# Performance work log

Measured on AMD Instinct MI355X. Metric: run time of the kernel, lower is better.

Reference implementation:

```python
import jax, jax.numpy as jnp
import numpy as np

HID = 256
POS_FREQ = 10
DIR_FREQ = 4
POS_ENC = 3 * (2 * POS_FREQ + 1)   # 63
DIR_ENC = 3 * (2 * DIR_FREQ + 1)   # 27
N_PTS = 262144


def _posenc(x, num_freq):
    freqs = (2.0 ** jnp.arange(num_freq)).astype(x.dtype)      # [F]
    xf = x[..., None, :] * freqs[:, None]                       # [..., F, D]
    sc = jnp.stack([jnp.sin(xf), jnp.cos(xf)], axis=-2)         # [..., F, 2, D]
    return jnp.concatenate([x, sc.reshape(*x.shape[:-1], -1)], axis=-1)


def _linear_init(key, fan_in, fan_out):
    kw, kb = jax.random.split(key)
    s = 1.0 / np.sqrt(fan_in)
    W = jax.random.uniform(kw, (fan_in, fan_out), jnp.float32, -s, s)
    b = jax.random.uniform(kb, (fan_out,), jnp.float32, -s, s)
    return W, b


def setup_inputs() -> dict:
    key = jax.random.key(0)
    ks = jax.random.split(key, 16)
    inp = {
        "positions": jax.random.normal(ks[0], (N_PTS, 3), jnp.float32),
        "directions": jax.random.normal(ks[1], (N_PTS, 3), jnp.float32),
    }
    W, b = _linear_init(ks[2], POS_ENC, HID)
    inp["W_in"], inp["b_in"] = W, b
    # 7 hidden layers; layer index 4 takes skip concat (HID + POS_ENC)
    for i in range(7):
        fan_in = HID + POS_ENC if i == 4 else HID
        W, b = _linear_init(ks[3 + i], fan_in, HID)
        inp[f"W_h{i}"], inp[f"b_h{i}"] = W, b
    W, b = _linear_init(ks[10], HID, HID + 1)
    inp["W_out"], inp["b_out"] = W, b
    W, b = _linear_init(ks[11], HID + DIR_ENC, HID // 2)
    inp["W_r1"], inp["b_r1"] = W, b
    W, b = _linear_init(ks[12], HID // 2, 3)
    inp["W_r2"], inp["b_r2"] = W, b
    return inp


def _forward(positions, directions, W_in, b_in, hidden_params, W_out, b_out,
             W_r1, b_r1, W_r2, b_r2):
    pe = _posenc(positions, POS_FREQ)    # [N, 63]
    de = _posenc(directions, DIR_FREQ)   # [N, 27]
    h = jax.nn.relu(pe @ W_in + b_in)    # [N, 256]
    for i, (W, b) in enumerate(hidden_params):
        if i == 4:
            h = jnp.concatenate([h, pe], axis=-1)  # skip connection [N, 319]
        h = jax.nn.relu(h @ W + b)
    out = h @ W_out + b_out                      # [N, 257]
    features = out[..., :HID]                    # [N, 256]
    density = jax.nn.relu(out[..., HID:HID + 1])  # [N, 1]
    rgb_in = jnp.concatenate([features, de], axis=-1)  # [N, 283]
    rgb = jax.nn.sigmoid(jax.nn.relu(rgb_in @ W_r1 + b_r1) @ W_r2 + b_r2)  # [N, 3]
    return rgb, density


def reference(positions, directions, W_in, b_in,
              W_h0, b_h0, W_h1, b_h1, W_h2, b_h2, W_h3, b_h3,
              W_h4, b_h4, W_h5, b_h5, W_h6, b_h6,
              W_out, b_out, W_r1, b_r1, W_r2, b_r2):
    hidden = [(W_h0, b_h0), (W_h1, b_h1), (W_h2, b_h2), (W_h3, b_h3),
              (W_h4, b_h4), (W_h5, b_h5), (W_h6, b_h6)]
    return _forward(positions, directions, W_in, b_in, hidden,
                    W_out, b_out, W_r1, b_r1, W_r2, b_r2)
```

## Files before the change

kernel.cpp:

```cpp
#include <hip/hip_runtime.h>
#include <math.h>

#define NPTS 262144
#define MT 128

typedef __attribute__((ext_vector_type(8))) short bf16x8;
typedef __attribute__((ext_vector_type(4))) float f32x4;
typedef __attribute__((ext_vector_type(16))) float f32x16;
typedef __attribute__((ext_vector_type(2))) unsigned int u32x2;

#if defined(__has_builtin)
#if __has_builtin(__builtin_amdgcn_cvt_pk_bf16_f32)
#define HAVE_CVT_PK_BF16 1
#endif
#endif

__device__ __forceinline__ short f2bf(float f) {
    union { float f; unsigned u; } v; v.f = f;
    unsigned r = v.u + 0x7fffu + ((v.u >> 16) & 1u);
    return (short)(r >> 16);
}
__device__ __forceinline__ unsigned pk2(float a, float b) {
#ifdef HAVE_CVT_PK_BF16
    auto r = __builtin_amdgcn_cvt_pk_bf16_f32(a, b);
    unsigned u; __builtin_memcpy(&u, &r, 4);
    return u;
#else
    return ((unsigned)(unsigned short)f2bf(a)) |
           ((unsigned)(unsigned short)f2bf(b) << 16);
#endif
}

__device__ __forceinline__ void barrier_lds() {
    asm volatile("s_waitcnt lgkmcnt(0)" ::: "memory");
    __builtin_amdgcn_s_barrier();
}

#define OFF_IN   0
#define SZ_IN    (64*256)
#define OFF_H0   (OFF_IN + SZ_IN)
#define SZ_H     (256*256)
#define OFF_H1   (OFF_H0 + SZ_H)
#define OFF_H2   (OFF_H1 + SZ_H)
#define OFF_H3   (OFF_H2 + SZ_H)
#define OFF_H4   (OFF_H3 + SZ_H)
#define SZ_H4    (320*256)
#define OFF_H5   (OFF_H4 + SZ_H4)
#define OFF_H6   (OFF_H5 + SZ_H)
#define OFF_OUT  (OFF_H6 + SZ_H)
#define SZ_OUTM  (256*256)
#define OFF_OUTD (OFF_OUT + SZ_OUTM)
#define SZ_OUTD  (256*16)
#define OFF_R1   (OFF_OUTD + SZ_OUTD)
#define SZ_R1    (288*128)
#define OFF_R2   (OFF_R1 + SZ_R1)
#define SZ_R2    (128*16)
#define WS_TOTAL (OFF_R2 + SZ_R2)

struct PrepP { const float* W[11]; short* ws; };

__global__ __launch_bounds__(256) void prep_all(PrepP pp) {
    int i = blockIdx.x * 256 + threadIdx.x;
    if (i >= WS_TOTAL) return;
    const int offs[13] = {OFF_IN, OFF_H0, OFF_H1, OFF_H2, OFF_H3, OFF_H4,
                          OFF_H5, OFF_H6, OFF_OUT, OFF_OUTD, OFF_R1, OFF_R2,
                          WS_TOTAL};
    const int wsrc[12] = {0,1,2,3,4,5,6,7,8,8,9,10};
    const int Ks[12]   = {63,256,256,256,256,319,256,256,256,256,283,128};
    const int Nsrc[12] = {256,256,256,256,256,256,256,256,257,257,128,3};
    int seg = 0;
    while (i >= offs[seg + 1]) seg++;
    int li = i - offs[seg];
    int j = li & 7, L = (li >> 3) & 63, tile = li >> 9;
    const float* W = pp.W[wsrc[seg]];
    float v = 0.f;
    if (seg == 9) {
        int k = tile * 32 + ((L >> 4) << 3) + j;
        if (k < 256 && (L & 15) == 0) v = W[k * 257 + 256];
    } else if (seg == 11) {
        int k = tile * 32 + ((L >> 4) << 3) + j;
        int n = L & 15;
        if (k < 128 && n < 3) v = W[k * 3 + n];
    } else {
        int nNb = (seg == 10) ? 4 : 8;
        int nb = tile % nNb, kt = tile / nNb;
        int k = kt * 16 + ((L >> 5) << 3) + j;
        int n = nb * 32 + (L & 31);
        if (k < Ks[seg]) v = W[k * Nsrc[seg] + n];
    }
    pp.ws[i] = f2bf(v);
}

struct Params {
    const float *pos, *dir;
    const float *b_in, *b_h0, *b_h1, *b_h2, *b_h3, *b_h4, *b_h5, *b_h6;
    const float *b_out, *b_r1, *b_r2;
    const short *w;
    float *out;
};

template<int NKT, int NNB, int TM, int MODE>
__device__ __forceinline__ void layer32(const short* __restrict__ Wsw,
                                        const short* __restrict__ Wd,
                                        const float* __restrict__ bias,
                                        short* X, float* dout, int p0,
                                        int nb, int mbB, int wave, int lane,
                                        bf16x8& a0io, bf16x8& a1io,
                                        const short* __restrict__ wpn, int nnbn) {
    const int l31 = lane & 31, hi = lane >> 5;
    const short* xb = X + hi * 1024 + (mbB * 32 + l31) * 8;
    const short* wp = Wsw + (size_t)(nb * 64 + lane) * 8;

    bf16x8 na0 = *(const bf16x8*)(wpn);
    bf16x8 na1 = *(const bf16x8*)(wpn + (size_t)nnbn * 512);

    bf16x8 a0 = a0io, a1 = a1io;

    barrier_lds();

    if (MODE == 1) {
        const int l15 = lane & 15, quad = lane >> 4;
        const short* xd = X + quad * 1024 + (wave * 16 + l15) * 8;
        f32x4 ad = (f32x4){0.f, 0.f, 0.f, 0.f};
#pragma unroll
        for (int kt = 0; kt < 8; ++kt) {
            bf16x8 b = *(const bf16x8*)(xd + kt * 4096);
            bf16x8 a = *(const bf16x8*)(Wd + (size_t)(kt * 64 + lane) * 8);
            ad = __builtin_amdgcn_mfma_f32_16x16x32_bf16(a, b, ad, 0, 0, 0);
        }
        if (quad == 0)
            dout[3 * NPTS + p0 + wave * 16 + l15] = fmaxf(ad[0] + bias[256], 0.f);
    }

    f32x16 acc[TM];
#pragma unroll
    for (int t = 0; t < TM; t++)
#pragma unroll
        for (int r = 0; r < 16; r++) acc[t][r] = 0.f;

    bf16x8 b_c[TM];
#pragma unroll
    for (int t = 0; t < TM; t++)
        b_c[t] = *(const bf16x8*)(xb + t * 256);

#pragma unroll
    for (int kt = 0; kt < NKT; ++kt) {
        bf16x8 b_n[TM], a_n;
        if (kt + 1 < NKT) {
#pragma unroll
            for (int t = 0; t < TM; t++)
                b_n[t] = *(const bf16x8*)(xb + (kt + 1) * 2048 + t * 256);
        }
        if (kt + 2 < NKT)
            a_n = *(const bf16x8*)(wp + (size_t)(kt + 2) * NNB * 512);
        if ((kt & 1) == 0) {
#pragma unroll
            for (int t = 0; t < TM; t++)
                acc[t] = __builtin_amdgcn_mfma_f32_32x32x16_bf16(a0, b_c[t], acc[t], 0, 0, 0);
        } else {
#pragma unroll
            for (int t = 0; t < TM; t++)
                acc[t] = __builtin_amdgcn_mfma_f32_32x32x16_bf16(a1, b_c[t], acc[t], 0, 0, 0);
        }
        if (kt + 2 < NKT) {
            if ((kt & 1) == 0) a0 = a_n; else a1 = a_n;
        }
        if (kt + 1 < NKT) {
#pragma unroll
            for (int t = 0; t < TM; t++) b_c[t] = b_n[t];
        }
    }

    barrier_lds();

#pragma unroll
    for (int t = 0; t < TM; t++) {
        const int m = (mbB + t) * 32 + l31;
#pragma unroll
        for (int rq = 0; rq < 4; rq++) {
            const int nbase = nb * 32 + rq * 8 + hi * 4;
            const f32x4 bv = *(const f32x4*)(bias + nbase);
            float v0 = acc[t][rq * 4 + 0] + bv[0];
            float v1 = acc[t][rq * 4 + 1] + bv[1];
            float v2 = acc[t][rq * 4 + 2] + bv[2];
            float v3 = acc[t][rq * 4 + 3] + bv[3];
            if (MODE == 0) {
                v0 = fmaxf(v0, 0.f); v1 = fmaxf(v1, 0.f);
                v2 = fmaxf(v2, 0.f); v3 = fmaxf(v3, 0.f);
            }
            u32x2 w; w[0] = pk2(v0, v1); w[1] = pk2(v2, v3);
            *(u32x2*)(X + (size_t)(nb * 4 + rq) * 1024 + m * 8 + hi * 4) = w;
        }
    }

    a0io = na0; a1io = na1;
}

__global__ __launch_bounds__(512, 4) void nerf_fused(Params P) {
    __shared__ __align__(16) short X[40 * 1024];
    const int tid = threadIdx.x;
    const int wave = tid >> 6, lane = tid & 63;
    const int p0 = blockIdx.x * MT;

    const size_t fo    = (size_t)(wave * 64 + lane) * 8;
    const size_t fo_r1 = (size_t)((wave & 3) * 64 + lane) * 8;
    const size_t fo_r2 = (size_t)lane * 8;

    bf16x8 a0 = *(const bf16x8*)(P.w + OFF_IN + fo);
    bf16x8 a1 = *(const bf16x8*)(P.w + OFF_IN + fo + 8 * 512);

    for (int i = tid; i < 128 * 8; i += 512) {
        const int pt = i & 127, g = i >> 7;
        const float x0 = P.pos[(p0 + pt) * 3 + 0];
        const float x1 = P.pos[(p0 + pt) * 3 + 1];
        const float x2 = P.pos[(p0 + pt) * 3 + 2];
        bf16x8 v;
#pragma unroll
        for (int j = 0; j < 8; j++) {
            const int d = g * 8 + j;
            float val = 0.f;
            if (d < 3) val = (d == 0) ? x0 : (d == 1) ? x1 : x2;
            else if (d < 63) {
                const int e = d - 3, f = e / 6, r = e % 6;
                const float x = (r % 3 == 0) ? x0 : (r % 3 == 1) ? x1 : x2;
                const float xf = x * (float)(1 << f);
                val = (r < 3) ? sinf(xf) : cosf(xf);
            }
            v[j] = f2bf(val);
        }
        *(bf16x8*)(X + ((size_t)g * 128 + pt) * 8) = v;
        *(bf16x8*)(X + ((size_t)(32 + g) * 128 + pt) * 8) = v;
    }

    bf16x8 de_v;
    const int ptD = tid & 127, gD = tid >> 7;
    {
        const float x0 = P.dir[(p0 + ptD) * 3 + 0];
        const float x1 = P.dir[(p0 + ptD) * 3 + 1];
        const float x2 = P.dir[(p0 + ptD) * 3 + 2];
#pragma unroll
        for (int j = 0; j < 8; j++) {
            const int d = gD * 8 + j;
            float val = 0.f;
            if (d < 3) val = (d == 0) ? x0 : (d == 1) ? x1 : x2;
            else if (d < 27) {
                const int e = d - 3, f = e / 6, r = e % 6;
                const float x = (r % 3 == 0) ? x0 : (r % 3 == 1) ? x1 : x2;
                const float xf = x * (float)(1 << f);
                val = (r < 3) ? sinf(xf) : cosf(xf);
            }
            de_v[j] = f2bf(val);
        }
    }

    layer32< 4, 8, 4, 0>(P.w + OFF_IN, nullptr, P.b_in, X, P.out, p0, wave, 0, wave, lane, a0, a1, P.w + OFF_H0 + fo, 8);
    layer32<16, 8, 4, 0>(P.w + OFF_H0, nullptr, P.b_h0, X, P.out, p0, wave, 0, wave, lane, a0, a1, P.w + OFF_H1 + fo, 8);
    layer32<16, 8, 4, 0>(P.w + OFF_H1, nullptr, P.b_h1, X, P.out, p0, wave, 0, wave, lane, a0, a1, P.w + OFF_H2 + fo, 8);
    layer32<16, 8, 4, 0>(P.w + OFF_H2, nullptr, P.b_h2, X, P.out, p0, wave, 0, wave, lane, a0, a1, P.w + OFF_H3 + fo, 8);
    layer32<16, 8, 4, 0>(P.w + OFF_H3, nullptr, P.b_h3, X, P.out, p0, wave, 0, wave, lane, a0, a1, P.w + OFF_H4 + fo, 8);
    layer32<20, 8, 4, 0>(P.w + OFF_H4, nullptr, P.b_h4, X, P.out, p0, wave, 0, wave, lane, a0, a1, P.w + OFF_H5 + fo, 8);

    *(bf16x8*)(X + ((size_t)(32 + gD) * 128 + ptD) * 8) = de_v;

    layer32<16, 8, 4, 0>(P.w + OFF_H5, nullptr, P.b_h5, X, P.out, p0, wave, 0, wave, lane, a0, a1, P.w + OFF_H6 + fo, 8);
    layer32<16, 8, 4, 0>(P.w + OFF_H6, nullptr, P.b_h6, X, P.out, p0, wave, 0, wave, lane, a0, a1, P.w + OFF_OUT + fo, 8);
    layer32<16, 8, 4, 1>(P.w + OFF_OUT, P.w + OFF_OUTD, P.b_out, X, P.out, p0, wave, 0, wave, lane, a0, a1, P.w + OFF_R1 + fo_r1, 4);

    layer32<18, 4, 2, 0>(P.w + OFF_R1, nullptr, P.b_r1, X, P.out, p0, wave & 3, (wave >> 2) * 2, wave, lane, a0, a1, P.w + OFF_R2 + fo_r2, 1);

    barrier_lds();
    {
        const int l15 = lane & 15, quad = lane >> 4;
        const short* xb = X + quad * 1024 + (wave * 16 + l15) * 8;
        bf16x8 a2 = *(const bf16x8*)(P.w + OFF_R2 + (size_t)(2 * 64 + lane) * 8);
        bf16x8 a3 = *(const bf16x8*)(P.w + OFF_R2 + (size_t)(3 * 64 + lane) * 8);
        f32x4 acc = (f32x4){0.f, 0.f, 0.f, 0.f};
        bf16x8 b0 = *(const bf16x8*)(xb);
        bf16x8 b1 = *(const bf16x8*)(xb + 4096);
        bf16x8 b2 = *(const bf16x8*)(xb + 8192);
        bf16x8 b3 = *(const bf16x8*)(xb + 12288);
        acc = __builtin_amdgcn_mfma_f32_16x16x32_bf16(a0, b0, acc, 0, 0, 0);
        acc = __builtin_amdgcn_mfma_f32_16x16x32_bf16(a1, b1, acc, 0, 0, 0);
        acc = __builtin_amdgcn_mfma_f32_16x16x32_bf16(a2, b2, acc, 0, 0, 0);
        acc = __builtin_amdgcn_mfma_f32_16x16x32_bf16(a3, b3, acc, 0, 0, 0);
        if (quad == 0) {
#pragma unroll
            for (int r = 0; r < 3; r++) {
                const float v = acc[r] + P.b_r2[r];
                P.out[(size_t)(p0 + wave * 16 + l15) * 3 + r] = 1.f / (1.f + expf(-v));
            }
        }
    }
}

extern "C" void kernel_launch(void* const* d_in, const int* in_sizes, int n_in,
                              void* d_out, int out_size, void* d_ws, size_t ws_size,
                              hipStream_t stream) {
    short* ws = (short*)d_ws;

    PrepP pp;
    pp.W[0]  = (const float*)d_in[2];
    pp.W[1]  = (const float*)d_in[4];
    pp.W[2]  = (const float*)d_in[6];
    pp.W[3]  = (const float*)d_in[8];
    pp.W[4]  = (const float*)d_in[10];
    pp.W[5]  = (const float*)d_in[12];
    pp.W[6]  = (const float*)d_in[14];
    pp.W[7]  = (const float*)d_in[16];
    pp.W[8]  = (const float*)d_in[18];
    pp.W[9]  = (const float*)d_in[20];
    pp.W[10] = (const float*)d_in[22];
    pp.ws = ws;
    hipLaunchKernelGGL(prep_all, dim3((WS_TOTAL + 255) / 256), dim3(256), 0, stream, pp);

    Params P;
    P.pos  = (const float*)d_in[0];
    P.dir  = (const float*)d_in[1];
    P.b_in = (const float*)d_in[3];
    P.b_h0 = (const float*)d_in[5];
    P.b_h1 = (const float*)d_in[7];
    P.b_h2 = (const float*)d_in[9];
    P.b_h3 = (const float*)d_in[11];
    P.b_h4 = (const float*)d_in[13];
    P.b_h5 = (const float*)d_in[15];
    P.b_h6 = (const float*)d_in[17];
    P.b_out = (const float*)d_in[19];
    P.b_r1 = (const float*)d_in[21];
    P.b_r2 = (const float*)d_in[23];
    P.w = ws;
    P.out = (float*)d_out;
    hipLaunchKernelGGL(nerf_fused, dim3(NPTS / MT), dim3(512), 0, stream, P);
}
```

Before: 403.7 us.

## Retile per-wave MLP work to 2x2 blocks of 32x32 output tiles

```diff
diff --git a/kernel.cpp b/kernel.cpp
--- a/kernel.cpp
+++ b/kernel.cpp
@@ -99,22 +99,23 @@
     float *out;
 };
 
-template<int NKT, int NNB, int TM, int MODE>
+template<int NKT, int NNB, int NS, int TM, int MODE>
 __device__ __forceinline__ void layer32(const short* __restrict__ Wsw,
                                         const short* __restrict__ Wd,
                                         const float* __restrict__ bias,
                                         short* X, float* dout, int p0,
-                                        int nb, int mbB, int wave, int lane,
-                                        bf16x8& a0io, bf16x8& a1io,
-                                        const short* __restrict__ wpn, int nnbn) {
+                                        int nbB, int mbB, int wave, int lane) {
     const int l31 = lane & 31, hi = lane >> 5;
     const short* xb = X + hi * 1024 + (mbB * 32 + l31) * 8;
-    const short* wp = Wsw + (size_t)(nb * 64 + lane) * 8;
-
-    bf16x8 na0 = *(const bf16x8*)(wpn);
-    bf16x8 na1 = *(const bf16x8*)(wpn + (size_t)nnbn * 512);
-
-    bf16x8 a0 = a0io, a1 = a1io;
+    const short* wp = Wsw + (size_t)(nbB * 64 + lane) * 8;
+
+    bf16x8 a0[NS], a1[NS];
+#pragma unroll
+    for (int s = 0; s < NS; s++)
+        a0[s] = *(const bf16x8*)(wp + (size_t)s * 512);
+#pragma unroll
+    for (int s = 0; s < NS; s++)
+        a1[s] = *(const bf16x8*)(wp + (size_t)(NNB + s) * 512);
 
     barrier_lds();
 
@@ -132,11 +133,13 @@
             dout[3 * NPTS + p0 + wave * 16 + l15] = fmaxf(ad[0] + bias[256], 0.f);
     }
 
-    f32x16 acc[TM];
-#pragma unroll
-    for (int t = 0; t < TM; t++)
-#pragma unroll
-        for (int r = 0; r < 16; r++) acc[t][r] = 0.f;
+    f32x16 acc[NS][TM];
+#pragma unroll
+    for (int s = 0; s < NS; s++)
+#pragma unroll
+        for (int t = 0; t < TM; t++)
+#pragma unroll
+            for (int r = 0; r < 16; r++) acc[s][t][r] = 0.f;
 
     bf16x8 b_c[TM];
 #pragma unroll
@@ -145,25 +148,38 @@
 
 #pragma unroll
     for (int kt = 0; kt < NKT; ++kt) {
-        bf16x8 b_n[TM], a_n;
+        bf16x8 b_n[TM], a_n[NS];
         if (kt + 1 < NKT) {
 #pragma unroll
             for (int t = 0; t < TM; t++)
                 b_n[t] = *(const bf16x8*)(xb + (kt + 1) * 2048 + t * 256);
         }
-        if (kt + 2 < NKT)
-            a_n = *(const bf16x8*)(wp + (size_t)(kt + 2) * NNB * 512);
+        if (kt + 2 < NKT) {
+#pragma unroll
+            for (int s = 0; s < NS; s++)
+                a_n[s] = *(const bf16x8*)(wp + (size_t)((kt + 2) * NNB + s) * 512);
+        }
         if ((kt & 1) == 0) {
 #pragma unroll
-            for (int t = 0; t < TM; t++)
-                acc[t] = __builtin_amdgcn_mfma_f32_32x32x16_bf16(a0, b_c[t], acc[t], 0, 0, 0);
+            for (int s = 0; s < NS; s++)
+#pragma unroll
+                for (int t = 0; t < TM; t++)
+                    acc[s][t] = __builtin_amdgcn_mfma_f32_32x32x16_bf16(a0[s], b_c[t], acc[s][t], 0, 0, 0);
         } else {
 #pragma unroll
-            for (int t = 0; t < TM; t++)
-                acc[t] = __builtin_amdgcn_mfma_f32_32x32x16_bf16(a1, b_c[t], acc[t], 0, 0, 0);
+            for (int s = 0; s < NS; s++)
+#pragma unroll
+                for (int t = 0; t < TM; t++)
+                    acc[s][t] = __builtin_amdgcn_mfma_f32_32x32x16_bf16(a1[s], b_c[t], acc[s][t], 0, 0, 0);
         }
         if (kt + 2 < NKT) {
-            if ((kt & 1) == 0) a0 = a_n; else a1 = a_n;
+            if ((kt & 1) == 0) {
+#pragma unroll
+                for (int s = 0; s < NS; s++) a0[s] = a_n[s];
+            } else {
+#pragma unroll
+                for (int s = 0; s < NS; s++) a1[s] = a_n[s];
+            }
         }
         if (kt + 1 < NKT) {
 #pragma unroll
@@ -174,26 +190,28 @@
     barrier_lds();
 
 #pragma unroll
-    for (int t = 0; t < TM; t++) {
-        const int m = (mbB + t) * 32 + l31;
-#pragma unroll
-        for (int rq = 0; rq < 4; rq++) {
-            const int nbase = nb * 32 + rq * 8 + hi * 4;
-            const f32x4 bv = *(const f32x4*)(bias + nbase);
-            float v0 = acc[t][rq * 4 + 0] + bv[0];
-            float v1 = acc[t][rq * 4 + 1] + bv[1];
-            float v2 = acc[t][rq * 4 + 2] + bv[2];
-            float v3 = acc[t][rq * 4 + 3] + bv[3];
-            if (MODE == 0) {
-                v0 = fmaxf(v0, 0.f); v1 = fmaxf(v1, 0.f);
-                v2 = fmaxf(v2, 0.f); v3 = fmaxf(v3, 0.f);
-            }
-            u32x2 w; w[0] = pk2(v0, v1); w[1] = pk2(v2, v3);
-            *(u32x2*)(X + (size_t)(nb * 4 + rq) * 1024 + m * 8 + hi * 4) = w;
-        }
-    }
-
-    a0io = na0; a1io = na1;
+    for (int s = 0; s < NS; s++) {
+        const int nb = nbB + s;
+#pragma unroll
+        for (int t = 0; t < TM; t++) {
+            const int m = (mbB + t) * 32 + l31;
+#pragma unroll
+            for (int rq = 0; rq < 4; rq++) {
+                const int nbase = nb * 32 + rq * 8 + hi * 4;
+                const f32x4 bv = *(const f32x4*)(bias + nbase);
+                float v0 = acc[s][t][rq * 4 + 0] + bv[0];
+                float v1 = acc[s][t][rq * 4 + 1] + bv[1];
+                float v2 = acc[s][t][rq * 4 + 2] + bv[2];
+                float v3 = acc[s][t][rq * 4 + 3] + bv[3];
+                if (MODE == 0) {
+                    v0 = fmaxf(v0, 0.f); v1 = fmaxf(v1, 0.f);
+                    v2 = fmaxf(v2, 0.f); v3 = fmaxf(v3, 0.f);
+                }
+                u32x2 w; w[0] = pk2(v0, v1); w[1] = pk2(v2, v3);
+                *(u32x2*)(X + (size_t)(nb * 4 + rq) * 1024 + m * 8 + hi * 4) = w;
+            }
+        }
+    }
 }
 
 __global__ __launch_bounds__(512, 4) void nerf_fused(Params P) {
@@ -202,12 +220,7 @@
     const int wave = tid >> 6, lane = tid & 63;
     const int p0 = blockIdx.x * MT;
 
-    const size_t fo    = (size_t)(wave * 64 + lane) * 8;
-    const size_t fo_r1 = (size_t)((wave & 3) * 64 + lane) * 8;
-    const size_t fo_r2 = (size_t)lane * 8;
-
-    bf16x8 a0 = *(const bf16x8*)(P.w + OFF_IN + fo);
-    bf16x8 a1 = *(const bf16x8*)(P.w + OFF_IN + fo + 8 * 512);
+    const int nbB_h = (wave & 3) * 2, mbB_h = (wave >> 2) * 2;
 
     for (int i = tid; i < 128 * 8; i += 512) {
         const int pt = i & 127, g = i >> 7;
@@ -232,12 +245,19 @@
         *(bf16x8*)(X + ((size_t)(32 + g) * 128 + pt) * 8) = v;
     }
 
-    bf16x8 de_v;
-    const int ptD = tid & 127, gD = tid >> 7;
+    layer32< 4, 8, 2, 2, 0>(P.w + OFF_IN, nullptr, P.b_in, X, P.out, p0, nbB_h, mbB_h, wave, lane);
+    layer32<16, 8, 2, 2, 0>(P.w + OFF_H0, nullptr, P.b_h0, X, P.out, p0, nbB_h, mbB_h, wave, lane);
+    layer32<16, 8, 2, 2, 0>(P.w + OFF_H1, nullptr, P.b_h1, X, P.out, p0, nbB_h, mbB_h, wave, lane);
+    layer32<16, 8, 2, 2, 0>(P.w + OFF_H2, nullptr, P.b_h2, X, P.out, p0, nbB_h, mbB_h, wave, lane);
+    layer32<16, 8, 2, 2, 0>(P.w + OFF_H3, nullptr, P.b_h3, X, P.out, p0, nbB_h, mbB_h, wave, lane);
+    layer32<20, 8, 2, 2, 0>(P.w + OFF_H4, nullptr, P.b_h4, X, P.out, p0, nbB_h, mbB_h, wave, lane);
+
     {
+        const int ptD = tid & 127, gD = tid >> 7;
         const float x0 = P.dir[(p0 + ptD) * 3 + 0];
         const float x1 = P.dir[(p0 + ptD) * 3 + 1];
         const float x2 = P.dir[(p0 + ptD) * 3 + 2];
+        bf16x8 de_v;
 #pragma unroll
         for (int j = 0; j < 8; j++) {
             const int d = gD * 8 + j;
@@ -251,27 +271,21 @@
             }
             de_v[j] = f2bf(val);
         }
-    }
-
-    layer32< 4, 8, 4, 0>(P.w + OFF_IN, nullptr, P.b_in, X, P.out, p0, wave, 0, wave, lane, a0, a1, P.w + OFF_H0 + fo, 8);
-    layer32<16, 8, 4, 0>(P.w + OFF_H0, nullptr, P.b_h0, X, P.out, p0, wave, 0, wave, lane, a0, a1, P.w + OFF_H1 + fo, 8);
-    layer32<16, 8, 4, 0>(P.w + OFF_H1, nullptr, P.b_h1, X, P.out, p0, wave, 0, wave, lane, a0, a1, P.w + OFF_H2 + fo, 8);
-    layer32<16, 8, 4, 0>(P.w + OFF_H2, nullptr, P.b_h2, X, P.out, p0, wave, 0, wave, lane, a0, a1, P.w + OFF_H3 + fo, 8);
-    layer32<16, 8, 4, 0>(P.w + OFF_H3, nullptr, P.b_h3, X, P.out, p0, wave, 0, wave, lane, a0, a1, P.w + OFF_H4 + fo, 8);
-    layer32<20, 8, 4, 0>(P.w + OFF_H4, nullptr, P.b_h4, X, P.out, p0, wave, 0, wave, lane, a0, a1, P.w + OFF_H5 + fo, 8);
-
-    *(bf16x8*)(X + ((size_t)(32 + gD) * 128 + ptD) * 8) = de_v;
-
-    layer32<16, 8, 4, 0>(P.w + OFF_H5, nullptr, P.b_h5, X, P.out, p0, wave, 0, wave, lane, a0, a1, P.w + OFF_H6 + fo, 8);
-    layer32<16, 8, 4, 0>(P.w + OFF_H6, nullptr, P.b_h6, X, P.out, p0, wave, 0, wave, lane, a0, a1, P.w + OFF_OUT + fo, 8);
-    layer32<16, 8, 4, 1>(P.w + OFF_OUT, P.w + OFF_OUTD, P.b_out, X, P.out, p0, wave, 0, wave, lane, a0, a1, P.w + OFF_R1 + fo_r1, 4);
-
-    layer32<18, 4, 2, 0>(P.w + OFF_R1, nullptr, P.b_r1, X, P.out, p0, wave & 3, (wave >> 2) * 2, wave, lane, a0, a1, P.w + OFF_R2 + fo_r2, 1);
+        *(bf16x8*)(X + ((size_t)(32 + gD) * 128 + ptD) * 8) = de_v;
+    }
+
+    layer32<16, 8, 2, 2, 0>(P.w + OFF_H5, nullptr, P.b_h5, X, P.out, p0, nbB_h, mbB_h, wave, lane);
+    layer32<16, 8, 2, 2, 0>(P.w + OFF_H6, nullptr, P.b_h6, X, P.out, p0, nbB_h, mbB_h, wave, lane);
+    layer32<16, 8, 2, 2, 1>(P.w + OFF_OUT, P.w + OFF_OUTD, P.b_out, X, P.out, p0, nbB_h, mbB_h, wave, lane);
+
+    layer32<18, 4, 2, 1, 0>(P.w + OFF_R1, nullptr, P.b_r1, X, P.out, p0, (wave & 1) * 2, wave >> 1, wave, lane);
 
     barrier_lds();
     {
         const int l15 = lane & 15, quad = lane >> 4;
         const short* xb = X + quad * 1024 + (wave * 16 + l15) * 8;
+        bf16x8 a0 = *(const bf16x8*)(P.w + OFF_R2 + (size_t)(0 * 64 + lane) * 8);
+        bf16x8 a1 = *(const bf16x8*)(P.w + OFF_R2 + (size_t)(1 * 64 + lane) * 8);
         bf16x8 a2 = *(const bf16x8*)(P.w + OFF_R2 + (size_t)(2 * 64 + lane) * 8);
         bf16x8 a3 = *(const bf16x8*)(P.w + OFF_R2 + (size_t)(3 * 64 + lane) * 8);
         f32x4 acc = (f32x4){0.f, 0.f, 0.f, 0.f};
```

Result: slower. 416.8 us (+3.2%).

## Halve point tile to 64 and drop cross-layer weight prefetch for higher occupancy

Applied to the files above, without the earlier changes.

```diff
diff --git a/kernel.cpp b/kernel.cpp
--- a/kernel.cpp
+++ b/kernel.cpp
@@ -2,7 +2,7 @@
 #include <math.h>
 
 #define NPTS 262144
-#define MT 128
+#define MT 64
 
 typedef __attribute__((ext_vector_type(8))) short bf16x8;
 typedef __attribute__((ext_vector_type(4))) float f32x4;
@@ -104,27 +104,23 @@
                                         const short* __restrict__ Wd,
                                         const float* __restrict__ bias,
                                         short* X, float* dout, int p0,
-                                        int nb, int mbB, int wave, int lane,
-                                        bf16x8& a0io, bf16x8& a1io,
-                                        const short* __restrict__ wpn, int nnbn) {
+                                        int nb, int mbB, int wave, int lane) {
     const int l31 = lane & 31, hi = lane >> 5;
-    const short* xb = X + hi * 1024 + (mbB * 32 + l31) * 8;
+    const short* xb = X + hi * 512 + (mbB * 32 + l31) * 8;
     const short* wp = Wsw + (size_t)(nb * 64 + lane) * 8;
 
-    bf16x8 na0 = *(const bf16x8*)(wpn);
-    bf16x8 na1 = *(const bf16x8*)(wpn + (size_t)nnbn * 512);
-
-    bf16x8 a0 = a0io, a1 = a1io;
+    bf16x8 a0 = *(const bf16x8*)(wp);
+    bf16x8 a1 = *(const bf16x8*)(wp + (size_t)NNB * 512);
 
     barrier_lds();
 
-    if (MODE == 1) {
+    if (MODE == 1 && wave < 4) {
         const int l15 = lane & 15, quad = lane >> 4;
-        const short* xd = X + quad * 1024 + (wave * 16 + l15) * 8;
+        const short* xd = X + quad * 512 + (wave * 16 + l15) * 8;
         f32x4 ad = (f32x4){0.f, 0.f, 0.f, 0.f};
 #pragma unroll
         for (int kt = 0; kt < 8; ++kt) {
-            bf16x8 b = *(const bf16x8*)(xd + kt * 4096);
+            bf16x8 b = *(const bf16x8*)(xd + kt * 2048);
             bf16x8 a = *(const bf16x8*)(Wd + (size_t)(kt * 64 + lane) * 8);
             ad = __builtin_amdgcn_mfma_f32_16x16x32_bf16(a, b, ad, 0, 0, 0);
         }
@@ -149,7 +145,7 @@
         if (kt + 1 < NKT) {
 #pragma unroll
             for (int t = 0; t < TM; t++)
-                b_n[t] = *(const bf16x8*)(xb + (kt + 1) * 2048 + t * 256);
+                b_n[t] = *(const bf16x8*)(xb + (kt + 1) * 1024 + t * 256);
         }
         if (kt + 2 < NKT)
             a_n = *(const bf16x8*)(wp + (size_t)(kt + 2) * NNB * 512);
@@ -189,28 +185,19 @@
                 v2 = fmaxf(v2, 0.f); v3 = fmaxf(v3, 0.f);
             }
             u32x2 w; w[0] = pk2(v0, v1); w[1] = pk2(v2, v3);
-            *(u32x2*)(X + (size_t)(nb * 4 + rq) * 1024 + m * 8 + hi * 4) = w;
-        }
-    }
-
-    a0io = na0; a1io = na1;
-}
-
-__global__ __launch_bounds__(512, 4) void nerf_fused(Params P) {
-    __shared__ __align__(16) short X[40 * 1024];
+            *(u32x2*)(X + (size_t)(nb * 4 + rq) * 512 + m * 8 + hi * 4) = w;
+        }
+    }
+}
+
+__global__ __launch_bounds__(512, 6) void nerf_fused(Params P) {
+    __shared__ __align__(16) short X[40 * 512];
     const int tid = threadIdx.x;
     const int wave = tid >> 6, lane = tid & 63;
     const int p0 = blockIdx.x * MT;
 
-    const size_t fo    = (size_t)(wave * 64 + lane) * 8;
-    const size_t fo_r1 = (size_t)((wave & 3) * 64 + lane) * 8;
-    const size_t fo_r2 = (size_t)lane * 8;
-
-    bf16x8 a0 = *(const bf16x8*)(P.w + OFF_IN + fo);
-    bf16x8 a1 = *(const bf16x8*)(P.w + OFF_IN + fo + 8 * 512);
-
-    for (int i = tid; i < 128 * 8; i += 512) {
-        const int pt = i & 127, g = i >> 7;
+    {
+        const int pt = tid & 63, g = tid >> 6;
         const float x0 = P.pos[(p0 + pt) * 3 + 0];
         const float x1 = P.pos[(p0 + pt) * 3 + 1];
         const float x2 = P.pos[(p0 + pt) * 3 + 2];
@@ -228,16 +215,23 @@
             }
             v[j] = f2bf(val);
         }
-        *(bf16x8*)(X + ((size_t)g * 128 + pt) * 8) = v;
-        *(bf16x8*)(X + ((size_t)(32 + g) * 128 + pt) * 8) = v;
-    }
-
-    bf16x8 de_v;
-    const int ptD = tid & 127, gD = tid >> 7;
-    {
+        *(bf16x8*)(X + ((size_t)g * 64 + pt) * 8) = v;
+        *(bf16x8*)(X + ((size_t)(32 + g) * 64 + pt) * 8) = v;
+    }
+
+    layer32< 4, 8, 2, 0>(P.w + OFF_IN, nullptr, P.b_in, X, P.out, p0, wave, 0, wave, lane);
+    layer32<16, 8, 2, 0>(P.w + OFF_H0, nullptr, P.b_h0, X, P.out, p0, wave, 0, wave, lane);
+    layer32<16, 8, 2, 0>(P.w + OFF_H1, nullptr, P.b_h1, X, P.out, p0, wave, 0, wave, lane);
+    layer32<16, 8, 2, 0>(P.w + OFF_H2, nullptr, P.b_h2, X, P.out, p0, wave, 0, wave, lane);
+    layer32<16, 8, 2, 0>(P.w + OFF_H3, nullptr, P.b_h3, X, P.out, p0, wave, 0, wave, lane);
+    layer32<20, 8, 2, 0>(P.w + OFF_H4, nullptr, P.b_h4, X, P.out, p0, wave, 0, wave, lane);
+
+    if (tid < 256) {
+        const int ptD = tid & 63, gD = tid >> 6;
         const float x0 = P.dir[(p0 + ptD) * 3 + 0];
         const float x1 = P.dir[(p0 + ptD) * 3 + 1];
         const float x2 = P.dir[(p0 + ptD) * 3 + 2];
+        bf16x8 de_v;
 #pragma unroll
         for (int j = 0; j < 8; j++) {
             const int d = gD * 8 + j;
@@ -251,34 +245,28 @@
             }
             de_v[j] = f2bf(val);
         }
-    }
-
-    layer32< 4, 8, 4, 0>(P.w + OFF_IN, nullptr, P.b_in, X, P.out, p0, wave, 0, wave, lane, a0, a1, P.w + OFF_H0 + fo, 8);
-    layer32<16, 8, 4, 0>(P.w + OFF_H0, nullptr, P.b_h0, X, P.out, p0, wave, 0, wave, lane, a0, a1, P.w + OFF_H1 + fo, 8);
-    layer32<16, 8, 4, 0>(P.w + OFF_H1, nullptr, P.b_h1, X, P.out, p0, wave, 0, wave, lane, a0, a1, P.w + OFF_H2 + fo, 8);
-    layer32<16, 8, 4, 0>(P.w + OFF_H2, nullptr, P.b_h2, X, P.out, p0, wave, 0, wave, lane, a0, a1, P.w + OFF_H3 + fo, 8);
-    layer32<16, 8, 4, 0>(P.w + OFF_H3, nullptr, P.b_h3, X, P.out, p0, wave, 0, wave, lane, a0, a1, P.w + OFF_H4 + fo, 8);
-    layer32<20, 8, 4, 0>(P.w + OFF_H4, nullptr, P.b_h4, X, P.out, p0, wave, 0, wave, lane, a0, a1, P.w + OFF_H5 + fo, 8);
-
-    *(bf16x8*)(X + ((size_t)(32 + gD) * 128 + ptD) * 8) = de_v;
-
-    layer32<16, 8, 4, 0>(P.w + OFF_H5, nullptr, P.b_h5, X, P.out, p0, wave, 0, wave, lane, a0, a1, P.w + OFF_H6 + fo, 8);
-    layer32<16, 8, 4, 0>(P.w + OFF_H6, nullptr, P.b_h6, X, P.out, p0, wave, 0, wave, lane, a0, a1, P.w + OFF_OUT + fo, 8);
-    layer32<16, 8, 4, 1>(P.w + OFF_OUT, P.w + OFF_OUTD, P.b_out, X, P.out, p0, wave, 0, wave, lane, a0, a1, P.w + OFF_R1 + fo_r1, 4);
-
-    layer32<18, 4, 2, 0>(P.w + OFF_R1, nullptr, P.b_r1, X, P.out, p0, wave & 3, (wave >> 2) * 2, wave, lane, a0, a1, P.w + OFF_R2 + fo_r2, 1);
+        *(bf16x8*)(X + ((size_t)(32 + gD) * 64 + ptD) * 8) = de_v;
+    }
+
+    layer32<16, 8, 2, 0>(P.w + OFF_H5, nullptr, P.b_h5, X, P.out, p0, wave, 0, wave, lane);
+    layer32<16, 8, 2, 0>(P.w + OFF_H6, nullptr, P.b_h6, X, P.out, p0, wave, 0, wave, lane);
+    layer32<16, 8, 2, 1>(P.w + OFF_OUT, P.w + OFF_OUTD, P.b_out, X, P.out, p0, wave, 0, wave, lane);
+
+    layer32<18, 4, 1, 0>(P.w + OFF_R1, nullptr, P.b_r1, X, P.out, p0, wave & 3, wave >> 2, wave, lane);
 
     barrier_lds();
-    {
+    if (wave < 4) {
         const int l15 = lane & 15, quad = lane >> 4;
-        const short* xb = X + quad * 1024 + (wave * 16 + l15) * 8;
+        const short* xb = X + quad * 512 + (wave * 16 + l15) * 8;
+        bf16x8 a0 = *(const bf16x8*)(P.w + OFF_R2 + (size_t)(0 * 64 + lane) * 8);
+        bf16x8 a1 = *(const bf16x8*)(P.w + OFF_R2 + (size_t)(1 * 64 + lane) * 8);
         bf16x8 a2 = *(const bf16x8*)(P.w + OFF_R2 + (size_t)(2 * 64 + lane) * 8);
         bf16x8 a3 = *(const bf16x8*)(P.w + OFF_R2 + (size_t)(3 * 64 + lane) * 8);
         f32x4 acc = (f32x4){0.f, 0.f, 0.f, 0.f};
         bf16x8 b0 = *(const bf16x8*)(xb);
-        bf16x8 b1 = *(const bf16x8*)(xb + 4096);
-        bf16x8 b2 = *(const bf16x8*)(xb + 8192);
-        bf16x8 b3 = *(const bf16x8*)(xb + 12288);
+        bf16x8 b1 = *(const bf16x8*)(xb + 2048);
+        bf16x8 b2 = *(const bf16x8*)(xb + 4096);
+        bf16x8 b3 = *(const bf16x8*)(xb + 6144);
         acc = __builtin_amdgcn_mfma_f32_16x16x32_bf16(a0, b0, acc, 0, 0, 0);
         acc = __builtin_amdgcn_mfma_f32_16x16x32_bf16(a1, b1, acc, 0, 0, 0);
         acc = __builtin_amdgcn_mfma_f32_16x16x32_bf16(a2, b2, acc, 0, 0, 0);
```

New measurement: 437.3 us. 1.08x slower.
